# Kernel tuning notes

Hardware: AMD Instinct MI355X
Metric: run time of the kernel (lower is better)

Reference implementation:

```python
import jax, jax.numpy as jnp
import numpy as np

B = 2048        # graphs per batch
NC = 81         # cells per sudoku
IN_C, HID = 10, 128
N_ACT, N_NUM, N_TECH = 4, 9, 10


def _sudoku_edges():
    idx = np.arange(NC).reshape(9, 9)
    adj = np.zeros((NC, NC), dtype=bool)
    for i in range(9):
        for j in range(9):
            n = idx[i, j]
            adj[n, idx[i, :]] = True
            adj[n, idx[:, j]] = True
            bi, bj = 3 * (i // 3), 3 * (j // 3)
            adj[n, idx[bi:bi + 3, bj:bj + 3].reshape(-1)] = True
            adj[n, n] = False
    src, dst = np.nonzero(adj)  # 1620 directed edges
    return np.stack([src, dst]).astype(np.int32)


def setup_inputs() -> dict:
    key = jax.random.key(0)
    ks = jax.random.split(key, 12)
    N = B * NC
    base = _sudoku_edges()                          # [2, 1620]
    offs = (np.arange(B, dtype=np.int32) * NC)      # [B]
    ei = (base[:, None, :] + offs[None, :, None]).reshape(2, -1)  # [2, B*1620]
    batch = np.repeat(np.arange(B, dtype=np.int32), NC)           # [N]

    def lin(k, fan_in, fan_out):
        s = 1.0 / np.sqrt(fan_in)
        return jax.random.uniform(k, (fan_in, fan_out), jnp.float32, -s, s)

    return {
        "x": jax.random.normal(ks[0], (N, IN_C), jnp.float32),
        "edge_index": jnp.asarray(ei),
        "batch": jnp.asarray(batch),
        "W1": lin(ks[1], IN_C, HID), "b1": jnp.zeros((HID,), jnp.float32),
        "W2": lin(ks[2], HID, HID),  "b2": jnp.zeros((HID,), jnp.float32),
        "Wa": lin(ks[3], HID, N_ACT),  "ba": jnp.zeros((N_ACT,), jnp.float32),
        "Wc": lin(ks[4], HID, NC),     "bc": jnp.zeros((NC,), jnp.float32),
        "Wn": lin(ks[5], HID, N_NUM),  "bn": jnp.zeros((N_NUM,), jnp.float32),
        "Wt": lin(ks[6], HID, N_TECH), "bt": jnp.zeros((N_TECH,), jnp.float32),
    }


def _gcn_conv(x, edge_index, W, b):
    n = x.shape[0]
    loop = jnp.arange(n, dtype=edge_index.dtype)
    src = jnp.concatenate([edge_index[0], loop])
    dst = jnp.concatenate([edge_index[1], loop])
    deg = jax.ops.segment_sum(jnp.ones_like(dst, jnp.float32), dst, num_segments=n)
    dinv = jax.lax.rsqrt(deg)            # deg >= 1 due to self-loops
    norm = dinv[src] * dinv[dst]         # [E+N]
    h = x @ W                            # [N, out]
    msg = h[src] * norm[:, None]         # gather + scale
    return jax.ops.segment_sum(msg, dst, num_segments=n) + b


def reference(x, edge_index, batch, W1, b1, W2, b2, Wa, ba, Wc, bc, Wn, bn, Wt, bt):
    h = jax.nn.relu(_gcn_conv(x, edge_index, W1, b1))
    h = jax.nn.relu(_gcn_conv(h, edge_index, W2, b2))
    # global mean pool over graphs
    sums = jax.ops.segment_sum(h, batch, num_segments=B)
    cnts = jax.ops.segment_sum(jnp.ones((h.shape[0],), h.dtype), batch, num_segments=B)
    pooled = sums / jnp.maximum(cnts, 1.0)[:, None]   # [B, HID]
    return (pooled @ Wa + ba, pooled @ Wc + bc, pooled @ Wn + bn, pooled @ Wt + bt)
```

## Files before the change

kernel.cpp:

```cpp
#include <hip/hip_runtime.h>
#include <hip/hip_bf16.h>

typedef __attribute__((ext_vector_type(8))) short bf16x8;
typedef __attribute__((ext_vector_type(4))) float f32x4;

__device__ __forceinline__ unsigned short f2b(float f) {
    __hip_bfloat16 h = __float2bfloat16(f);
    return __builtin_bit_cast(unsigned short, h);
}
__device__ __forceinline__ float b2f(unsigned short u) {
    unsigned v = ((unsigned)u) << 16;
    return __builtin_bit_cast(float, v);
}
__device__ __forceinline__ float ldf(const void* p, int idx, bool f32) {
    return f32 ? ((const float*)p)[idx] : b2f(((const unsigned short*)p)[idx]);
}
__device__ __forceinline__ unsigned short ldb(const void* p, int idx, bool f32) {
    return f32 ? f2b(((const float*)p)[idx]) : ((const unsigned short*)p)[idx];
}
__device__ __forceinline__ int swz(int row, int col) {
    return row * 128 + (((col >> 3) ^ (row & 7)) << 3) + (col & 7);
}

__device__ __forceinline__ bool sniff_f32(const void* x) {
    const unsigned* p = (const unsigned*)x;
    int wild = 0;
#pragma unroll
    for (int i = 0; i < 16; ++i) {
        unsigned e = (p[i] >> 7) & 0xFF;
        wild += (e != 0 && (e < 0x68 || e > 0x90)) ? 1 : 0;
    }
    return wild > 8;
}

#define WS_B1F    16
#define WS_B2F    528
#define WS_BHF    1040
#define WS_W1R    1536
#define WS_W2R    9728
#define WS_SR     42496
#define WS_WH     60928

__global__ void k_repack(const void* __restrict__ x,
                         const void* __restrict__ W1, const void* __restrict__ b1,
                         const void* __restrict__ W2, const void* __restrict__ b2,
                         const void* __restrict__ Wa, const void* __restrict__ ba,
                         const void* __restrict__ Wc, const void* __restrict__ bc,
                         const void* __restrict__ Wn, const void* __restrict__ bn,
                         const void* __restrict__ Wt, const void* __restrict__ bt,
                         char* __restrict__ ws) {
    const bool f32 = sniff_f32(x);
    int idx = blockIdx.x * blockDim.x + threadIdx.x;
    if (idx < 4096) {
        int f = idx >> 5, k = idx & 31;
        unsigned short v = (k < 10) ? ldb(W1, k * 128 + f, f32) : (unsigned short)0;
        ((unsigned short*)(ws + WS_W1R))[idx] = v;
        return;
    }
    idx -= 4096;
    if (idx < 16384) {
        int f = idx >> 7, k = idx & 127;
        ((unsigned short*)(ws + WS_W2R))[idx] = ldb(W2, k * 128 + f, f32);
        return;
    }
    idx -= 16384;
    if (idx < 9216) {
        int fi = idx >> 9, rem = idx & 511;
        int lane = rem >> 3, j = rem & 7;
        int mi = fi / 3, kc = fi - mi * 3;
        int node = mi * 16 + (lane & 15);
        int cell = kc * 32 + ((lane >> 4) << 3) + j;
        bool adj = false;
        if (node < 81 && cell < 81) {
            int ni = node / 9, nj = node % 9;
            int ci = cell / 9, cj = cell % 9;
            adj = (ni == ci) || (nj == cj) ||
                  ((ni / 3 == ci / 3) && (nj / 3 == cj / 3));
        }
        ((unsigned short*)(ws + WS_SR))[idx] = adj ? (unsigned short)0x3F80 : (unsigned short)0;
        return;
    }
    idx -= 9216;
    if (idx < 13312) {
        int o = idx >> 7, f = idx & 127;
        const void* W; int oo, dim;
        if (o < 4)       { W = Wa; oo = o;      dim = 4;  }
        else if (o < 85) { W = Wc; oo = o - 4;  dim = 81; }
        else if (o < 94) { W = Wn; oo = o - 85; dim = 9;  }
        else             { W = Wt; oo = o - 94; dim = 10; }
        ((float*)(ws + WS_WH))[idx] = ldf(W, f * dim + oo, f32);
        return;
    }
    idx -= 13312;
    if (idx < 360) {
        float v;
        if (idx < 128)      v = ldf(b1, idx, f32);
        else if (idx < 256) v = ldf(b2, idx - 128, f32);
        else {
            int o = idx - 256;
            if (o < 4)       v = ldf(ba, o, f32);
            else if (o < 85) v = ldf(bc, o - 4, f32);
            else if (o < 94) v = ldf(bn, o - 85, f32);
            else             v = ldf(bt, o - 94, f32);
        }
        if (idx < 128)      ((float*)(ws + WS_B1F))[idx] = v;
        else if (idx < 256) ((float*)(ws + WS_B2F))[idx - 128] = v;
        else                ((float*)(ws + WS_BHF))[idx - 256] = v;
    }
}

__global__ __launch_bounds__(256, 2) void sudoku_gnn(
    const void* __restrict__ x, const char* __restrict__ ws,
    void* __restrict__ out, int nB)
{
    __shared__ __attribute__((aligned(16))) unsigned short sA[16384];
    __shared__ __attribute__((aligned(16))) unsigned short sB[16384];
    __shared__ __attribute__((aligned(16))) unsigned int   xs2[1632];
    __shared__ float sPoolPart[2][256];
    __shared__ float sPool[2][128];

    const bool f32 = sniff_f32(x);
    const unsigned short* w1r = (const unsigned short*)(ws + WS_W1R);
    const unsigned short* w2r = (const unsigned short*)(ws + WS_W2R);
    const unsigned short* sr  = (const unsigned short*)(ws + WS_SR);
    const float* b1f = (const float*)(ws + WS_B1F);
    const float* b2f = (const float*)(ws + WS_B2F);
    const float* bhf = (const float*)(ws + WS_BHF);
    const float* whf = (const float*)(ws + WS_WH);

    const int tid  = threadIdx.x;
    const int wave = tid >> 6;
    const int lane = tid & 63;
    const int ln15 = lane & 15;
    const int q    = lane >> 4;
    const int k0   = q * 8;
    const int mtb  = (wave & 1) * 3;
    const int nb   = (wave & 1) * 48;
    const int fb   = (wave >> 1) * 64;
    const int g0   = blockIdx.x * 2;
    const int g1   = g0 + 1;
    const bool hasB = (g1 < nB);
    const float inv21 = 1.0f / 21.0f;
    unsigned short* const buf[2] = {sA, sB};

    {
        const int words = f32 ? 810 : 405;
        const int tot = words * (hasB ? 2 : 1);
        const unsigned int* src = (const unsigned int*)x + (size_t)g0 * words;
        for (int i = tid; i < tot; i += 256) xs2[i] = src[i];
    }

    bf16x8 sfr[3][3];
#pragma unroll
    for (int kc = 0; kc < 3; ++kc)
#pragma unroll
        for (int jt = 0; jt < 3; ++jt)
            sfr[kc][jt] = *(const bf16x8*)&sr[(((mtb + jt) * 3 + kc) * 64 + lane) * 8];
    bf16x8 w1f[4];
#pragma unroll
    for (int nt = 0; nt < 4; ++nt)
        w1f[nt] = *(const bf16x8*)&w1r[(fb + nt * 16 + ln15) * 32 + k0];

    __syncthreads();

    bf16x8 xf[2][3];
#pragma unroll
    for (int gg = 0; gg < 2; ++gg)
#pragma unroll
        for (int mt = 0; mt < 3; ++mt) {
            int node = (mtb + mt) * 16 + ln15;
            bf16x8 v = {0, 0, 0, 0, 0, 0, 0, 0};
            if (node < 81) {
                int base = gg * 810 + node * 10;
                if (q == 0) {
#pragma unroll
                    for (int jj = 0; jj < 8; ++jj)
                        v[jj] = (short)(f32 ? f2b(((const float*)xs2)[base + jj])
                                            : ((const unsigned short*)xs2)[base + jj]);
                } else if (q == 1) {
#pragma unroll
                    for (int jj = 0; jj < 2; ++jj)
                        v[jj] = (short)(f32 ? f2b(((const float*)xs2)[base + 8 + jj])
                                            : ((const unsigned short*)xs2)[base + 8 + jj]);
                }
            }
            xf[gg][mt] = v;
        }

    const f32x4 z4 = {0.f, 0.f, 0.f, 0.f};
    f32x4 acc[2][3][4];

#pragma unroll
    for (int gg = 0; gg < 2; ++gg)
#pragma unroll
        for (int mt = 0; mt < 3; ++mt)
#pragma unroll
            for (int nt = 0; nt < 4; ++nt)
                acc[gg][mt][nt] = __builtin_amdgcn_mfma_f32_16x16x32_bf16(xf[gg][mt], w1f[nt], z4, 0, 0, 0);
#pragma unroll
    for (int gg = 0; gg < 2; ++gg)
#pragma unroll
        for (int mt = 0; mt < 3; ++mt)
#pragma unroll
            for (int nt = 0; nt < 4; ++nt) {
                int f = fb + nt * 16 + ln15;
                int nodeb = (mtb + mt) * 16 + q * 4;
                unsigned lo = (unsigned)f2b(acc[gg][mt][nt][0]) | ((unsigned)f2b(acc[gg][mt][nt][1]) << 16);
                unsigned hi = (unsigned)f2b(acc[gg][mt][nt][2]) | ((unsigned)f2b(acc[gg][mt][nt][3]) << 16);
                *(uint2*)&buf[gg][swz(f, nodeb)] = make_uint2(lo, hi);
            }
    __syncthreads();

#pragma unroll
    for (int gg = 0; gg < 2; ++gg)
#pragma unroll
        for (int a = 0; a < 3; ++a)
#pragma unroll
            for (int b = 0; b < 4; ++b) acc[gg][a][b] = z4;
#pragma unroll
    for (int kc = 0; kc < 3; ++kc) {
        bf16x8 a4[2][4];
#pragma unroll
        for (int gg = 0; gg < 2; ++gg)
#pragma unroll
            for (int at = 0; at < 4; ++at)
                a4[gg][at] = *(const bf16x8*)&buf[gg][swz(fb + at * 16 + ln15, kc * 32 + k0)];
#pragma unroll
        for (int gg = 0; gg < 2; ++gg)
#pragma unroll
            for (int at = 0; at < 4; ++at)
#pragma unroll
                for (int jt = 0; jt < 3; ++jt)
                    acc[gg][jt][at] = __builtin_amdgcn_mfma_f32_16x16x32_bf16(a4[gg][at], sfr[kc][jt], acc[gg][jt][at], 0, 0, 0);
    }
    __syncthreads();
#pragma unroll
    for (int gg = 0; gg < 2; ++gg)
#pragma unroll
        for (int at = 0; at < 4; ++at) {
            float4 bv = *(const float4*)&b1f[fb + at * 16 + q * 4];
#pragma unroll
            for (int jt = 0; jt < 3; ++jt) {
                int node = nb + jt * 16 + ln15;
                float v0 = fmaxf(acc[gg][jt][at][0] * inv21 + bv.x, 0.0f);
                float v1 = fmaxf(acc[gg][jt][at][1] * inv21 + bv.y, 0.0f);
                float v2 = fmaxf(acc[gg][jt][at][2] * inv21 + bv.z, 0.0f);
                float v3 = fmaxf(acc[gg][jt][at][3] * inv21 + bv.w, 0.0f);
                unsigned lo = (unsigned)f2b(v0) | ((unsigned)f2b(v1) << 16);
                unsigned hi = (unsigned)f2b(v2) | ((unsigned)f2b(v3) << 16);
                *(uint2*)&buf[gg][swz(node, fb + at * 16 + q * 4)] = make_uint2(lo, hi);
            }
        }
    __syncthreads();

#pragma unroll
    for (int gg = 0; gg < 2; ++gg)
#pragma unroll
        for (int a = 0; a < 3; ++a)
#pragma unroll
            for (int b = 0; b < 4; ++b) acc[gg][a][b] = z4;
#pragma unroll
    for (int kc = 0; kc < 4; ++kc) {
        bf16x8 w2f[4];
#pragma unroll
        for (int nt = 0; nt < 4; ++nt)
            w2f[nt] = *(const bf16x8*)&w2r[(fb + nt * 16 + ln15) * 128 + kc * 32 + k0];
        bf16x8 a3[2][3];
#pragma unroll
        for (int gg = 0; gg < 2; ++gg)
#pragma unroll
            for (int mt = 0; mt < 3; ++mt)
                a3[gg][mt] = *(const bf16x8*)&buf[gg][swz((mtb + mt) * 16 + ln15, kc * 32 + k0)];
#pragma unroll
        for (int gg = 0; gg < 2; ++gg)
#pragma unroll
            for (int mt = 0; mt < 3; ++mt)
#pragma unroll
                for (int nt = 0; nt < 4; ++nt)
                    acc[gg][mt][nt] = __builtin_amdgcn_mfma_f32_16x16x32_bf16(a3[gg][mt], w2f[nt], acc[gg][mt][nt], 0, 0, 0);
    }
    __syncthreads();
#pragma unroll
    for (int gg = 0; gg < 2; ++gg)
#pragma unroll
        for (int mt = 0; mt < 3; ++mt)
#pragma unroll
            for (int nt = 0; nt < 4; ++nt) {
                int f = fb + nt * 16 + ln15;
                int nodeb = (mtb + mt) * 16 + q * 4;
                unsigned lo = (unsigned)f2b(acc[gg][mt][nt][0]) | ((unsigned)f2b(acc[gg][mt][nt][1]) << 16);
                unsigned hi = (unsigned)f2b(acc[gg][mt][nt][2]) | ((unsigned)f2b(acc[gg][mt][nt][3]) << 16);
                *(uint2*)&buf[gg][swz(f, nodeb)] = make_uint2(lo, hi);
            }
    __syncthreads();

#pragma unroll
    for (int gg = 0; gg < 2; ++gg)
#pragma unroll
        for (int a = 0; a < 3; ++a)
#pragma unroll
            for (int b = 0; b < 4; ++b) acc[gg][a][b] = z4;
#pragma unroll
    for (int kc = 0; kc < 3; ++kc) {
        bf16x8 a4[2][4];
#pragma unroll
        for (int gg = 0; gg < 2; ++gg)
#pragma unroll
            for (int at = 0; at < 4; ++at)
                a4[gg][at] = *(const bf16x8*)&buf[gg][swz(fb + at * 16 + ln15, kc * 32 + k0)];
#pragma unroll
        for (int gg = 0; gg < 2; ++gg)
#pragma unroll
            for (int at = 0; at < 4; ++at)
#pragma unroll
                for (int jt = 0; jt < 3; ++jt)
                    acc[gg][jt][at] = __builtin_amdgcn_mfma_f32_16x16x32_bf16(a4[gg][at], sfr[kc][jt], acc[gg][jt][at], 0, 0, 0);
    }
#pragma unroll
    for (int gg = 0; gg < 2; ++gg)
#pragma unroll
        for (int at = 0; at < 4; ++at) {
            float4 bv = *(const float4*)&b2f[fb + at * 16 + q * 4];
            float s0 = 0.f, s1 = 0.f, s2 = 0.f, s3 = 0.f;
#pragma unroll
            for (int jt = 0; jt < 3; ++jt) {
                int node = nb + jt * 16 + ln15;
                if (node < 81) {
                    s0 += fmaxf(acc[gg][jt][at][0] * inv21 + bv.x, 0.0f);
                    s1 += fmaxf(acc[gg][jt][at][1] * inv21 + bv.y, 0.0f);
                    s2 += fmaxf(acc[gg][jt][at][2] * inv21 + bv.z, 0.0f);
                    s3 += fmaxf(acc[gg][jt][at][3] * inv21 + bv.w, 0.0f);
                }
            }
#pragma unroll
            for (int off = 1; off < 16; off <<= 1) {
                s0 += __shfl_xor(s0, off);
                s1 += __shfl_xor(s1, off);
                s2 += __shfl_xor(s2, off);
                s3 += __shfl_xor(s3, off);
            }
            if (ln15 == 0) {
                float4 v = {s0, s1, s2, s3};
                *(float4*)&sPoolPart[gg][(wave & 1) * 128 + fb + at * 16 + q * 4] = v;
            }
        }
    __syncthreads();
    {
        int gg = tid >> 7;
        int f  = tid & 127;
        sPool[gg][f] = (sPoolPart[gg][f] + sPoolPart[gg][128 + f]) / 81.0f;
    }
    __syncthreads();

    {
        int gg = tid >> 7;
        int o  = tid & 127;
        int g  = gg ? g1 : g0;
        if (o < 104 && (gg == 0 || hasB)) {
            float a = bhf[o];
            const float4* wrow = (const float4*)(whf + o * 128);
            const float4* sp4  = (const float4*)sPool[gg];
#pragma unroll 8
            for (int i = 0; i < 32; ++i) {
                float4 wv = wrow[i];
                float4 pv = sp4[i];
                a += pv.x * wv.x + pv.y * wv.y + pv.z * wv.z + pv.w * wv.w;
            }
            int oo; size_t off;
            if (o < 4)       { oo = o;      off = (size_t)g * 4 + oo; }
            else if (o < 85) { oo = o - 4;  off = (size_t)nB * 4  + (size_t)g * 81 + oo; }
            else if (o < 94) { oo = o - 85; off = (size_t)nB * 85 + (size_t)g * 9  + oo; }
            else             { oo = o - 94; off = (size_t)nB * 94 + (size_t)g * 10 + oo; }
            if (f32) ((float*)out)[off] = a;
            else     ((unsigned short*)out)[off] = f2b(a);
        }
    }
}

extern "C" void kernel_launch(void* const* d_in, const int* in_sizes, int n_in,
                              void* d_out, int out_size, void* d_ws, size_t ws_size,
                              hipStream_t stream) {
    const void* x  = d_in[0];
    int nB = in_sizes[2] / 81;
    if (nB <= 0) return;

    char* ws = (char*)d_ws;
    hipLaunchKernelGGL(k_repack, dim3(170), dim3(256), 0, stream,
                       x, d_in[3], d_in[4], d_in[5], d_in[6],
                       d_in[7], d_in[8], d_in[9], d_in[10],
                       d_in[11], d_in[12], d_in[13], d_in[14], ws);
    hipLaunchKernelGGL(sudoku_gnn, dim3((nB + 1) / 2), dim3(256), 0, stream,
                       x, (const char*)ws, d_out, nB);
}
```

Before: 144.1 us.

## Process one graph per block instead of two to raise occupancy

The fused GNN kernel now handles a single sudoku graph per 256-thread block instead of two. That halves shared memory (one 32KB buffer instead of two), halves the accumulator register arrays, and raises the launch-bounds occupancy hint from 2 to 4 blocks per CU. The grid doubles to nB blocks. In exchange, the per-block setup cost is paid twice as often: loading the adjacency and W1 fragments, the barriers, and the per-block head GEMV. Each block also has half as many independent MFMAs between barriers to hide latency.

```diff
diff --git a/kernel.cpp b/kernel.cpp
--- a/kernel.cpp
+++ b/kernel.cpp
@@ -109,15 +109,14 @@
     }
 }
 
-__global__ __launch_bounds__(256, 2) void sudoku_gnn(
+__global__ __launch_bounds__(256, 4) void sudoku_gnn(
     const void* __restrict__ x, const char* __restrict__ ws,
     void* __restrict__ out, int nB)
 {
     __shared__ __attribute__((aligned(16))) unsigned short sA[16384];
-    __shared__ __attribute__((aligned(16))) unsigned short sB[16384];
-    __shared__ __attribute__((aligned(16))) unsigned int   xs2[1632];
-    __shared__ float sPoolPart[2][256];
-    __shared__ float sPool[2][128];
+    __shared__ __attribute__((aligned(16))) unsigned int   xs[816];
+    __shared__ float sPoolPart[256];
+    __shared__ float sPool[128];
 
     const bool f32 = sniff_f32(x);
     const unsigned short* w1r = (const unsigned short*)(ws + WS_W1R);
@@ -137,17 +136,13 @@
     const int mtb  = (wave & 1) * 3;
     const int nb   = (wave & 1) * 48;
     const int fb   = (wave >> 1) * 64;
-    const int g0   = blockIdx.x * 2;
-    const int g1   = g0 + 1;
-    const bool hasB = (g1 < nB);
+    const int g    = blockIdx.x;
     const float inv21 = 1.0f / 21.0f;
-    unsigned short* const buf[2] = {sA, sB};
 
     {
         const int words = f32 ? 810 : 405;
-        const int tot = words * (hasB ? 2 : 1);
-        const unsigned int* src = (const unsigned int*)x + (size_t)g0 * words;
-        for (int i = tid; i < tot; i += 256) xs2[i] = src[i];
+        const unsigned int* src = (const unsigned int*)x + (size_t)g * words;
+        for (int i = tid; i < words; i += 256) xs[i] = src[i];
     }
 
     bf16x8 sfr[3][3];
@@ -163,203 +158,169 @@
 
     __syncthreads();
 
-    bf16x8 xf[2][3];
-#pragma unroll
-    for (int gg = 0; gg < 2; ++gg)
-#pragma unroll
-        for (int mt = 0; mt < 3; ++mt) {
-            int node = (mtb + mt) * 16 + ln15;
-            bf16x8 v = {0, 0, 0, 0, 0, 0, 0, 0};
-            if (node < 81) {
-                int base = gg * 810 + node * 10;
-                if (q == 0) {
-#pragma unroll
-                    for (int jj = 0; jj < 8; ++jj)
-                        v[jj] = (short)(f32 ? f2b(((const float*)xs2)[base + jj])
-                                            : ((const unsigned short*)xs2)[base + jj]);
-                } else if (q == 1) {
-#pragma unroll
-                    for (int jj = 0; jj < 2; ++jj)
-                        v[jj] = (short)(f32 ? f2b(((const float*)xs2)[base + 8 + jj])
-                                            : ((const unsigned short*)xs2)[base + 8 + jj]);
-                }
+    bf16x8 xf[3];
+#pragma unroll
+    for (int mt = 0; mt < 3; ++mt) {
+        int node = (mtb + mt) * 16 + ln15;
+        bf16x8 v = {0, 0, 0, 0, 0, 0, 0, 0};
+        if (node < 81) {
+            int base = node * 10;
+            if (q == 0) {
+#pragma unroll
+                for (int jj = 0; jj < 8; ++jj)
+                    v[jj] = (short)(f32 ? f2b(((const float*)xs)[base + jj])
+                                        : ((const unsigned short*)xs)[base + jj]);
+            } else if (q == 1) {
+#pragma unroll
+                for (int jj = 0; jj < 2; ++jj)
+                    v[jj] = (short)(f32 ? f2b(((const float*)xs)[base + 8 + jj])
+                                        : ((const unsigned short*)xs)[base + 8 + jj]);
             }
-            xf[gg][mt] = v;
-        }
+        }
+        xf[mt] = v;
+    }
 
     const f32x4 z4 = {0.f, 0.f, 0.f, 0.f};
-    f32x4 acc[2][3][4];
-
-#pragma unroll
-    for (int gg = 0; gg < 2; ++gg)
-#pragma unroll
-        for (int mt = 0; mt < 3; ++mt)
-#pragma unroll
-            for (int nt = 0; nt < 4; ++nt)
-                acc[gg][mt][nt] = __builtin_amdgcn_mfma_f32_16x16x32_bf16(xf[gg][mt], w1f[nt], z4, 0, 0, 0);
-#pragma unroll
-    for (int gg = 0; gg < 2; ++gg)
-#pragma unroll
-        for (int mt = 0; mt < 3; ++mt)
-#pragma unroll
-            for (int nt = 0; nt < 4; ++nt) {
-                int f = fb + nt * 16 + ln15;
-                int nodeb = (mtb + mt) * 16 + q * 4;
-                unsigned lo = (unsigned)f2b(acc[gg][mt][nt][0]) | ((unsigned)f2b(acc[gg][mt][nt][1]) << 16);
-                unsigned hi = (unsigned)f2b(acc[gg][mt][nt][2]) | ((unsigned)f2b(acc[gg][mt][nt][3]) << 16);
-                *(uint2*)&buf[gg][swz(f, nodeb)] = make_uint2(lo, hi);
-            }
-    __syncthreads();
-
-#pragma unroll
-    for (int gg = 0; gg < 2; ++gg)
-#pragma unroll
-        for (int a = 0; a < 3; ++a)
-#pragma unroll
-            for (int b = 0; b < 4; ++b) acc[gg][a][b] = z4;
+    f32x4 acc[3][4];
+
+#pragma unroll
+    for (int mt = 0; mt < 3; ++mt)
+#pragma unroll
+        for (int nt = 0; nt < 4; ++nt)
+            acc[mt][nt] = __builtin_amdgcn_mfma_f32_16x16x32_bf16(xf[mt], w1f[nt], z4, 0, 0, 0);
+#pragma unroll
+    for (int mt = 0; mt < 3; ++mt)
+#pragma unroll
+        for (int nt = 0; nt < 4; ++nt) {
+            int f = fb + nt * 16 + ln15;
+            int nodeb = (mtb + mt) * 16 + q * 4;
+            unsigned lo = (unsigned)f2b(acc[mt][nt][0]) | ((unsigned)f2b(acc[mt][nt][1]) << 16);
+            unsigned hi = (unsigned)f2b(acc[mt][nt][2]) | ((unsigned)f2b(acc[mt][nt][3]) << 16);
+            *(uint2*)&sA[swz(f, nodeb)] = make_uint2(lo, hi);
+        }
+    __syncthreads();
+
+#pragma unroll
+    for (int a = 0; a < 3; ++a)
+#pragma unroll
+        for (int b = 0; b < 4; ++b) acc[a][b] = z4;
 #pragma unroll
     for (int kc = 0; kc < 3; ++kc) {
-        bf16x8 a4[2][4];
-#pragma unroll
-        for (int gg = 0; gg < 2; ++gg)
-#pragma unroll
-            for (int at = 0; at < 4; ++at)
-                a4[gg][at] = *(const bf16x8*)&buf[gg][swz(fb + at * 16 + ln15, kc * 32 + k0)];
-#pragma unroll
-        for (int gg = 0; gg < 2; ++gg)
-#pragma unroll
-            for (int at = 0; at < 4; ++at)
-#pragma unroll
-                for (int jt = 0; jt < 3; ++jt)
-                    acc[gg][jt][at] = __builtin_amdgcn_mfma_f32_16x16x32_bf16(a4[gg][at], sfr[kc][jt], acc[gg][jt][at], 0, 0, 0);
-    }
-    __syncthreads();
-#pragma unroll
-    for (int gg = 0; gg < 2; ++gg)
-#pragma unroll
-        for (int at = 0; at < 4; ++at) {
-            float4 bv = *(const float4*)&b1f[fb + at * 16 + q * 4];
-#pragma unroll
-            for (int jt = 0; jt < 3; ++jt) {
-                int node = nb + jt * 16 + ln15;
-                float v0 = fmaxf(acc[gg][jt][at][0] * inv21 + bv.x, 0.0f);
-                float v1 = fmaxf(acc[gg][jt][at][1] * inv21 + bv.y, 0.0f);
-                float v2 = fmaxf(acc[gg][jt][at][2] * inv21 + bv.z, 0.0f);
-                float v3 = fmaxf(acc[gg][jt][at][3] * inv21 + bv.w, 0.0f);
-                unsigned lo = (unsigned)f2b(v0) | ((unsigned)f2b(v1) << 16);
-                unsigned hi = (unsigned)f2b(v2) | ((unsigned)f2b(v3) << 16);
-                *(uint2*)&buf[gg][swz(node, fb + at * 16 + q * 4)] = make_uint2(lo, hi);
-            }
-        }
-    __syncthreads();
-
-#pragma unroll
-    for (int gg = 0; gg < 2; ++gg)
-#pragma unroll
-        for (int a = 0; a < 3; ++a)
-#pragma unroll
-            for (int b = 0; b < 4; ++b) acc[gg][a][b] = z4;
+        bf16x8 a4[4];
+#pragma unroll
+        for (int at = 0; at < 4; ++at)
+            a4[at] = *(const bf16x8*)&sA[swz(fb + at * 16 + ln15, kc * 32 + k0)];
+#pragma unroll
+        for (int at = 0; at < 4; ++at)
+#pragma unroll
+            for (int jt = 0; jt < 3; ++jt)
+                acc[jt][at] = __builtin_amdgcn_mfma_f32_16x16x32_bf16(a4[at], sfr[kc][jt], acc[jt][at], 0, 0, 0);
+    }
+    __syncthreads();
+#pragma unroll
+    for (int at = 0; at < 4; ++at) {
+        float4 bv = *(const float4*)&b1f[fb + at * 16 + q * 4];
+#pragma unroll
+        for (int jt = 0; jt < 3; ++jt) {
+            int node = nb + jt * 16 + ln15;
+            float v0 = fmaxf(acc[jt][at][0] * inv21 + bv.x, 0.0f);
+            float v1 = fmaxf(acc[jt][at][1] * inv21 + bv.y, 0.0f);
+            float v2 = fmaxf(acc[jt][at][2] * inv21 + bv.z, 0.0f);
+            float v3 = fmaxf(acc[jt][at][3] * inv21 + bv.w, 0.0f);
+            unsigned lo = (unsigned)f2b(v0) | ((unsigned)f2b(v1) << 16);
+            unsigned hi = (unsigned)f2b(v2) | ((unsigned)f2b(v3) << 16);
+            *(uint2*)&sA[swz(node, fb + at * 16 + q * 4)] = make_uint2(lo, hi);
+        }
+    }
+    __syncthreads();
+
+#pragma unroll
+    for (int a = 0; a < 3; ++a)
+#pragma unroll
+        for (int b = 0; b < 4; ++b) acc[a][b] = z4;
 #pragma unroll
     for (int kc = 0; kc < 4; ++kc) {
         bf16x8 w2f[4];
 #pragma unroll
         for (int nt = 0; nt < 4; ++nt)
             w2f[nt] = *(const bf16x8*)&w2r[(fb + nt * 16 + ln15) * 128 + kc * 32 + k0];
-        bf16x8 a3[2][3];
-#pragma unroll
-        for (int gg = 0; gg < 2; ++gg)
-#pragma unroll
-            for (int mt = 0; mt < 3; ++mt)
-                a3[gg][mt] = *(const bf16x8*)&buf[gg][swz((mtb + mt) * 16 + ln15, kc * 32 + k0)];
-#pragma unroll
-        for (int gg = 0; gg < 2; ++gg)
-#pragma unroll
-            for (int mt = 0; mt < 3; ++mt)
-#pragma unroll
-                for (int nt = 0; nt < 4; ++nt)
-                    acc[gg][mt][nt] = __builtin_amdgcn_mfma_f32_16x16x32_bf16(a3[gg][mt], w2f[nt], acc[gg][mt][nt], 0, 0, 0);
-    }
-    __syncthreads();
-#pragma unroll
-    for (int gg = 0; gg < 2; ++gg)
+        bf16x8 a3[3];
 #pragma unroll
         for (int mt = 0; mt < 3; ++mt)
-#pragma unroll
-            for (int nt = 0; nt < 4; ++nt) {
-                int f = fb + nt * 16 + ln15;
-                int nodeb = (mtb + mt) * 16 + q * 4;
-                unsigned lo = (unsigned)f2b(acc[gg][mt][nt][0]) | ((unsigned)f2b(acc[gg][mt][nt][1]) << 16);
-                unsigned hi = (unsigned)f2b(acc[gg][mt][nt][2]) | ((unsigned)f2b(acc[gg][mt][nt][3]) << 16);
-                *(uint2*)&buf[gg][swz(f, nodeb)] = make_uint2(lo, hi);
+            a3[mt] = *(const bf16x8*)&sA[swz((mtb + mt) * 16 + ln15, kc * 32 + k0)];
+#pragma unroll
+        for (int mt = 0; mt < 3; ++mt)
+#pragma unroll
+            for (int nt = 0; nt < 4; ++nt)
+                acc[mt][nt] = __builtin_amdgcn_mfma_f32_16x16x32_bf16(a3[mt], w2f[nt], acc[mt][nt], 0, 0, 0);
+    }
+    __syncthreads();
+#pragma unroll
+    for (int mt = 0; mt < 3; ++mt)
+#pragma unroll
+        for (int nt = 0; nt < 4; ++nt) {
+            int f = fb + nt * 16 + ln15;
+            int nodeb = (mtb + mt) * 16 + q * 4;
+            unsigned lo = (unsigned)f2b(acc[mt][nt][0]) | ((unsigned)f2b(acc[mt][nt][1]) << 16);
+            unsigned hi = (unsigned)f2b(acc[mt][nt][2]) | ((unsigned)f2b(acc[mt][nt][3]) << 16);
+            *(uint2*)&sA[swz(f, nodeb)] = make_uint2(lo, hi);
+        }
+    __syncthreads();
+
+#pragma unroll
+    for (int a = 0; a < 3; ++a)
+#pragma unroll
+        for (int b = 0; b < 4; ++b) acc[a][b] = z4;
+#pragma unroll
+    for (int kc = 0; kc < 3; ++kc) {
+        bf16x8 a4[4];
+#pragma unroll
+        for (int at = 0; at < 4; ++at)
+            a4[at] = *(const bf16x8*)&sA[swz(fb + at * 16 + ln15, kc * 32 + k0)];
+#pragma unroll
+        for (int at = 0; at < 4; ++at)
+#pragma unroll
+            for (int jt = 0; jt < 3; ++jt)
+                acc[jt][at] = __builtin_amdgcn_mfma_f32_16x16x32_bf16(a4[at], sfr[kc][jt], acc[jt][at], 0, 0, 0);
+    }
+#pragma unroll
+    for (int at = 0; at < 4; ++at) {
+        float4 bv = *(const float4*)&b2f[fb + at * 16 + q * 4];
+        float s0 = 0.f, s1 = 0.f, s2 = 0.f, s3 = 0.f;
+#pragma unroll
+        for (int jt = 0; jt < 3; ++jt) {
+            int node = nb + jt * 16 + ln15;
+            if (node < 81) {
+                s0 += fmaxf(acc[jt][at][0] * inv21 + bv.x, 0.0f);
+                s1 += fmaxf(acc[jt][at][1] * inv21 + bv.y, 0.0f);
+                s2 += fmaxf(acc[jt][at][2] * inv21 + bv.z, 0.0f);
+                s3 += fmaxf(acc[jt][at][3] * inv21 + bv.w, 0.0f);
             }
-    __syncthreads();
-
-#pragma unroll
-    for (int gg = 0; gg < 2; ++gg)
-#pragma unroll
-        for (int a = 0; a < 3; ++a)
-#pragma unroll
-            for (int b = 0; b < 4; ++b) acc[gg][a][b] = z4;
-#pragma unroll
-    for (int kc = 0; kc < 3; ++kc) {
-        bf16x8 a4[2][4];
-#pragma unroll
-        for (int gg = 0; gg < 2; ++gg)
-#pragma unroll
-            for (int at = 0; at < 4; ++at)
-                a4[gg][at] = *(const bf16x8*)&buf[gg][swz(fb + at * 16 + ln15, kc * 32 + k0)];
-#pragma unroll
-        for (int gg = 0; gg < 2; ++gg)
-#pragma unroll
-            for (int at = 0; at < 4; ++at)
-#pragma unroll
-                for (int jt = 0; jt < 3; ++jt)
-                    acc[gg][jt][at] = __builtin_amdgcn_mfma_f32_16x16x32_bf16(a4[gg][at], sfr[kc][jt], acc[gg][jt][at], 0, 0, 0);
-    }
-#pragma unroll
-    for (int gg = 0; gg < 2; ++gg)
-#pragma unroll
-        for (int at = 0; at < 4; ++at) {
-            float4 bv = *(const float4*)&b2f[fb + at * 16 + q * 4];
-            float s0 = 0.f, s1 = 0.f, s2 = 0.f, s3 = 0.f;
-#pragma unroll
-            for (int jt = 0; jt < 3; ++jt) {
-                int node = nb + jt * 16 + ln15;
-                if (node < 81) {
-                    s0 += fmaxf(acc[gg][jt][at][0] * inv21 + bv.x, 0.0f);
-                    s1 += fmaxf(acc[gg][jt][at][1] * inv21 + bv.y, 0.0f);
-                    s2 += fmaxf(acc[gg][jt][at][2] * inv21 + bv.z, 0.0f);
-                    s3 += fmaxf(acc[gg][jt][at][3] * inv21 + bv.w, 0.0f);
-                }
-            }
-#pragma unroll
-            for (int off = 1; off < 16; off <<= 1) {
-                s0 += __shfl_xor(s0, off);
-                s1 += __shfl_xor(s1, off);
-                s2 += __shfl_xor(s2, off);
-                s3 += __shfl_xor(s3, off);
-            }
-            if (ln15 == 0) {
-                float4 v = {s0, s1, s2, s3};
-                *(float4*)&sPoolPart[gg][(wave & 1) * 128 + fb + at * 16 + q * 4] = v;
-            }
-        }
-    __syncthreads();
+        }
+#pragma unroll
+        for (int off = 1; off < 16; off <<= 1) {
+            s0 += __shfl_xor(s0, off);
+            s1 += __shfl_xor(s1, off);
+            s2 += __shfl_xor(s2, off);
+            s3 += __shfl_xor(s3, off);
+        }
+        if (ln15 == 0) {
+            float4 v = {s0, s1, s2, s3};
+            *(float4*)&sPoolPart[(wave & 1) * 128 + fb + at * 16 + q * 4] = v;
+        }
+    }
+    __syncthreads();
+    if (tid < 128) {
+        sPool[tid] = (sPoolPart[tid] + sPoolPart[128 + tid]) / 81.0f;
+    }
+    __syncthreads();
+
     {
-        int gg = tid >> 7;
-        int f  = tid & 127;
-        sPool[gg][f] = (sPoolPart[gg][f] + sPoolPart[gg][128 + f]) / 81.0f;
-    }
-    __syncthreads();
-
-    {
-        int gg = tid >> 7;
-        int o  = tid & 127;
-        int g  = gg ? g1 : g0;
-        if (o < 104 && (gg == 0 || hasB)) {
+        int o = tid;
+        if (o < 104) {
             float a = bhf[o];
             const float4* wrow = (const float4*)(whf + o * 128);
-            const float4* sp4  = (const float4*)sPool[gg];
+            const float4* sp4  = (const float4*)sPool;
 #pragma unroll 8
             for (int i = 0; i < 32; ++i) {
                 float4 wv = wrow[i];
@@ -389,6 +350,6 @@
                        x, d_in[3], d_in[4], d_in[5], d_in[6],
                        d_in[7], d_in[8], d_in[9], d_in[10],
                        d_in[11], d_in[12], d_in[13], d_in[14], ws);
-    hipLaunchKernelGGL(sudoku_gnn, dim3((nB + 1) / 2), dim3(256), 0, stream,
+    hipLaunchKernelGGL(sudoku_gnn, dim3(nB), dim3(256), 0, stream,
                        x, (const char*)ws, d_out, nB);
 }
```

Result: no change. 145.4 us (+0.9%).
